# Optimization experiments

Hardware: AMD Instinct MI355X
Metric: run time of the kernel (lower is better)

## Reference

```python
import jax, jax.numpy as jnp
import numpy as np

B, CIN, COUT = 2, 64, 64
D, H, W = 8, 32, 32
KD = KH = KW = 3
K = KD * KH * KW  # 27
STRIDE, PAD, DIL = 1, 1, 1
DOUT = (D + 2 * PAD - DIL * (KD - 1) - 1) // STRIDE + 1
HOUT = (H + 2 * PAD - DIL * (KH - 1) - 1) // STRIDE + 1
WOUT = (W + 2 * PAD - DIL * (KW - 1) - 1) // STRIDE + 1


def setup_inputs() -> dict:
    key = jax.random.key(0)
    k1, k2, k3, k4 = jax.random.split(key, 4)
    x = jax.random.normal(k1, (B, CIN, D, H, W), dtype=jnp.float32)
    offset = jax.random.normal(k2, (B, 3 * K, DOUT, HOUT, WOUT), dtype=jnp.float32)
    weight = jax.random.normal(k3, (COUT, CIN, KD, KH, KW), dtype=jnp.float32) * 0.05
    bias = jax.random.normal(k4, (COUT,), dtype=jnp.float32) * 0.1
    return {"x": x, "offset": offset, "weight": weight, "bias": bias}


def _trilinear_sample(xb, zd, zh, zw):
    # xb: [C, D, H, W]; zd/zh/zw: [K, P] float sampling coords (zero padding outside)
    Dd, Hh, Ww = xb.shape[1], xb.shape[2], xb.shape[3]
    d0 = jnp.floor(zd); h0 = jnp.floor(zh); w0 = jnp.floor(zw)
    fd = zd - d0; fh = zh - h0; fw = zw - w0
    d0i = d0.astype(jnp.int32); h0i = h0.astype(jnp.int32); w0i = w0.astype(jnp.int32)
    acc = jnp.zeros((xb.shape[0],) + zd.shape, dtype=xb.dtype)
    for dd in (0, 1):
        for dh in (0, 1):
            for dw in (0, 1):
                di = d0i + dd; hi = h0i + dh; wi = w0i + dw
                wgt = ((fd if dd else 1.0 - fd) * (fh if dh else 1.0 - fh)
                       * (fw if dw else 1.0 - fw))
                valid = ((di >= 0) & (di < Dd) & (hi >= 0) & (hi < Hh)
                         & (wi >= 0) & (wi < Ww)).astype(xb.dtype)
                v = xb[:, jnp.clip(di, 0, Dd - 1), jnp.clip(hi, 0, Hh - 1),
                       jnp.clip(wi, 0, Ww - 1)]  # [C, K, P]
                acc = acc + v * (wgt * valid)[None]
    return acc


def _deform_conv3d(x, offset, weight, bias):
    Bb = x.shape[0]
    P = DOUT * HOUT * WOUT
    # kernel taps
    kd, kh, kw = jnp.unravel_index(jnp.arange(K), (KD, KH, KW))
    # output grid
    od, oh, ow = jnp.meshgrid(jnp.arange(DOUT), jnp.arange(HOUT), jnp.arange(WOUT), indexing="ij")
    base_d = (od[None] * STRIDE - PAD + kd[:, None, None, None] * DIL).astype(jnp.float32)  # [K,Do,Ho,Wo]
    base_h = (oh[None] * STRIDE - PAD + kh[:, None, None, None] * DIL).astype(jnp.float32)
    base_w = (ow[None] * STRIDE - PAD + kw[:, None, None, None] * DIL).astype(jnp.float32)
    off = offset.reshape(Bb, K, 3, DOUT, HOUT, WOUT)  # per-tap (dd, dh, dw)
    zd = (base_d[None] + off[:, :, 0]).reshape(Bb, K, P)
    zh = (base_h[None] + off[:, :, 1]).reshape(Bb, K, P)
    zw = (base_w[None] + off[:, :, 2]).reshape(Bb, K, P)
    sampled = jax.vmap(_trilinear_sample)(x, zd, zh, zw)  # [B, C, K, P]
    wmat = weight.reshape(COUT, CIN, K)
    out = jnp.einsum("bckp,ock->bop", sampled, wmat)  # [B, COUT, P]
    out = out + bias[None, :, None]
    return out.reshape(Bb, COUT, DOUT, HOUT, WOUT)


def reference(x, offset, weight, bias):
    return _deform_conv3d(x, offset, weight, bias)
```

## Files before the change

### kernel.cpp

```cpp
#include <hip/hip_runtime.h>
#include <hip/hip_bf16.h>


#define BB    2
#define CINC  64
#define COUTC 64
#define DDEP  8
#define HGT   32
#define WID   32
#define KK    27
#define KGRP  9
#define KPB   3
#define PP    8192
#define TP    64
#define LDW   72

typedef short s16x8 __attribute__((ext_vector_type(8)));
typedef float f32x4 __attribute__((ext_vector_type(4)));
typedef unsigned short u16x8 __attribute__((ext_vector_type(8)));

__device__ __forceinline__ unsigned short f2bf(float f) {
    unsigned u = __builtin_bit_cast(unsigned, f);
    u += 0x7FFFu + ((u >> 16) & 1u);
    return (unsigned short)(u >> 16);
}

__device__ __forceinline__ unsigned pack2bf(float lo, float hi) {
    return (unsigned)f2bf(lo) | ((unsigned)f2bf(hi) << 16);
}

__device__ __forceinline__ float bfu_lo(unsigned v) {
    return __builtin_bit_cast(float, v << 16);
}
__device__ __forceinline__ float bfu_hi(unsigned v) {
    return __builtin_bit_cast(float, v & 0xFFFF0000u);
}

__global__ void pre_kernel(const float* __restrict__ x, const float* __restrict__ w,
                           unsigned short* __restrict__ xt, unsigned short* __restrict__ wt) {
    __shared__ float sT[64][65];
    const int t    = threadIdx.x;
    const int lane = t & 63;
    const int wv   = t >> 6;
    const int half = lane >> 5;
    const int c2   = lane & 31;
    int blk = blockIdx.x;
    if (blk < 256) {
        int b  = blk >> 7;
        int s0 = (blk & 127) * 64;
        #pragma unroll
        for (int i = 0; i < 16; ++i) {
            int c = wv * 16 + i;
            sT[c][lane] = x[(size_t)(b * CINC + c) * PP + s0 + lane];
        }
        __syncthreads();
        #pragma unroll
        for (int i = 0; i < 8; ++i) {
            int s = wv * 16 + 2 * i + half;
            unsigned pk = pack2bf(sT[2 * c2][s], sT[2 * c2 + 1][s]);
            *(unsigned*)&xt[(size_t)(b * PP + s0 + s) * 64 + 2 * c2] = pk;
        }
    } else {
        int id = (blk - 256) * 256 + t;
        if (id < KK * COUTC * CINC) {
            int c = id & 63;
            int o = (id >> 6) & 63;
            int k = id >> 12;
            wt[id] = f2bf(w[(o * CINC + c) * KK + k]);
        }
    }
}

__device__ __forceinline__ void acc8(float* s, int4 v, float wg) {
    s[0] += wg * bfu_lo((unsigned)v.x); s[1] += wg * bfu_hi((unsigned)v.x);
    s[2] += wg * bfu_lo((unsigned)v.y); s[3] += wg * bfu_hi((unsigned)v.y);
    s[4] += wg * bfu_lo((unsigned)v.z); s[5] += wg * bfu_hi((unsigned)v.z);
    s[6] += wg * bfu_lo((unsigned)v.w); s[7] += wg * bfu_hi((unsigned)v.w);
}

__global__ __launch_bounds__(256, 3) void deform_kernel(
    const unsigned short* __restrict__ xt, const float* __restrict__ off,
    const unsigned short* __restrict__ wt, const float* __restrict__ bias,
    float* __restrict__ out)
{
    __shared__ unsigned short sW[KPB * COUTC * LDW] __attribute__((aligned(16)));
    __shared__ unsigned short sS[TP * LDW]          __attribute__((aligned(16)));
    __shared__ u16x8 sIdx[KPB][TP] __attribute__((aligned(16)));
    __shared__ float sCf[KPB][TP][8] __attribute__((aligned(16)));

    const int t    = threadIdx.x;
    const int lane = t & 63;
    const int wv   = t >> 6;
    const int b    = blockIdx.x >> 7;
    const int p0   = (blockIdx.x & 127) * TP;
    const int kg   = blockIdx.y;

    const unsigned short* xb = xt + (size_t)b * PP * 64;

    f32x4 acc[4];
    #pragma unroll
    for (int f = 0; f < 4; ++f) acc[f] = (f32x4)0.0f;

    const int n0 = lane & 15;
    const int q  = lane >> 4;

    {
        const unsigned short* wk = wt + (kg * KPB) * (COUTC * CINC);
        #pragma unroll
        for (int j = 0; j < 6; ++j) {
            int idx = j * 2048 + t * 8;
            int kl  = idx >> 12;
            int rem = idx & 4095;
            *(s16x8*)&sW[kl * (COUTC * LDW) + (rem >> 6) * LDW + (rem & 63)] =
                *(const s16x8*)(wk + idx);
        }
    }

    if (t < KPB * TP) {
        int kl = t >> 6;
        int k  = kg * KPB + kl;
        int pl = t & 63;
        int pp = p0 + pl;
        int ow = pp & 31;
        int oh = (pp >> 5) & 31;
        int od = pp >> 10;
        int kd = k / 9;
        int kh = (k - kd * 9) / 3;
        int kw = k - kd * 9 - kh * 3;
        const float* ob = off + (size_t)(b * (3 * KK) + 3 * k) * PP + pp;
        float zd = (float)(od - 1 + kd) + ob[0];
        float zh = (float)(oh - 1 + kh) + ob[PP];
        float zw = (float)(ow - 1 + kw) + ob[2 * PP];

        float fdf = floorf(zd); int d0 = (int)fdf; float fd = zd - fdf;
        float fhf = floorf(zh); int h0 = (int)fhf; float fh = zh - fhf;
        float fwf = floorf(zw); int w0 = (int)fwf; float fw = zw - fwf;

        float Bd0 = (d0 >= 0     && d0 < DDEP)     ? 1.0f - fd : 0.0f;
        float Bd1 = (d0 + 1 >= 0 && d0 + 1 < DDEP) ? fd        : 0.0f;
        float Ch0 = (h0 >= 0     && h0 < HGT)      ? 1.0f - fh : 0.0f;
        float Ch1 = (h0 + 1 >= 0 && h0 + 1 < HGT)  ? fh        : 0.0f;
        float Aw0 = (w0 >= 0     && w0 < WID)      ? 1.0f - fw : 0.0f;
        float Aw1 = (w0 + 1 >= 0 && w0 + 1 < WID)  ? fw        : 0.0f;
        int dc0 = min(max(d0, 0), DDEP - 1);
        int dc1 = min(max(d0 + 1, 0), DDEP - 1);
        int hc0 = min(max(h0, 0), HGT - 1);
        int hc1 = min(max(h0 + 1, 0), HGT - 1);
        int wc0 = min(max(w0, 0), WID - 1);
        int wc1 = min(max(w0 + 1, 0), WID - 1);

        int dh0 = (dc0 * HGT + hc0) * WID;
        int dh1 = (dc0 * HGT + hc1) * WID;
        int dh2 = (dc1 * HGT + hc0) * WID;
        int dh3 = (dc1 * HGT + hc1) * WID;
        u16x8 iv;
        iv[0] = (unsigned short)(dh0 + wc0);
        iv[1] = (unsigned short)(dh1 + wc0);
        iv[2] = (unsigned short)(dh2 + wc0);
        iv[3] = (unsigned short)(dh3 + wc0);
        iv[4] = (unsigned short)(dh0 + wc1);
        iv[5] = (unsigned short)(dh1 + wc1);
        iv[6] = (unsigned short)(dh2 + wc1);
        iv[7] = (unsigned short)(dh3 + wc1);
        sIdx[kl][pl] = iv;
        float bc0 = Bd0 * Ch0, bc1 = Bd0 * Ch1, bc2 = Bd1 * Ch0, bc3 = Bd1 * Ch1;
        sCf[kl][pl][0] = bc0 * Aw0;
        sCf[kl][pl][1] = bc1 * Aw0;
        sCf[kl][pl][2] = bc2 * Aw0;
        sCf[kl][pl][3] = bc3 * Aw0;
        sCf[kl][pl][4] = bc0 * Aw1;
        sCf[kl][pl][5] = bc1 * Aw1;
        sCf[kl][pl][6] = bc2 * Aw1;
        sCf[kl][pl][7] = bc3 * Aw1;
    }
    __syncthreads();

    const int coff = (lane & 7) * 8;
    #pragma unroll 1
    for (int kl = 0; kl < KPB; ++kl) {
        #pragma unroll
        for (int jp = 0; jp < 2; ++jp) {
            int prow = 16 * wv + 8 * jp + (lane >> 3);
            u16x8  iv = sIdx[kl][prow];
            float4 u0 = *(const float4*)&sCf[kl][prow][0];
            float4 u1 = *(const float4*)&sCf[kl][prow][4];
            const int4 v0 = *(const int4*)(xb + ((int)iv[0] << 6) + coff);
            const int4 v1 = *(const int4*)(xb + ((int)iv[1] << 6) + coff);
            const int4 v2 = *(const int4*)(xb + ((int)iv[2] << 6) + coff);
            const int4 v3 = *(const int4*)(xb + ((int)iv[3] << 6) + coff);
            const int4 v4 = *(const int4*)(xb + ((int)iv[4] << 6) + coff);
            const int4 v5 = *(const int4*)(xb + ((int)iv[5] << 6) + coff);
            const int4 v6 = *(const int4*)(xb + ((int)iv[6] << 6) + coff);
            const int4 v7 = *(const int4*)(xb + ((int)iv[7] << 6) + coff);
            float s[8] = {0, 0, 0, 0, 0, 0, 0, 0};
            acc8(s, v0, u0.x);
            acc8(s, v1, u0.y);
            acc8(s, v2, u0.z);
            acc8(s, v3, u0.w);
            acc8(s, v4, u1.x);
            acc8(s, v5, u1.y);
            acc8(s, v6, u1.z);
            acc8(s, v7, u1.w);
            int4 pk;
            pk.x = (int)pack2bf(s[0], s[1]);
            pk.y = (int)pack2bf(s[2], s[3]);
            pk.z = (int)pack2bf(s[4], s[5]);
            pk.w = (int)pack2bf(s[6], s[7]);
            *(int4*)&sS[prow * LDW + coff] = pk;
        }
        {
            s16x8 b0 = *(const s16x8*)&sS[(16 * wv + n0) * LDW +      8 * q];
            s16x8 b1 = *(const s16x8*)&sS[(16 * wv + n0) * LDW + 32 + 8 * q];
            const unsigned short* sWk = &sW[kl * (COUTC * LDW)];
            #pragma unroll
            for (int f = 0; f < 4; ++f) {
                s16x8 a0 = *(const s16x8*)&sWk[(16 * f + n0) * LDW +      8 * q];
                s16x8 a1 = *(const s16x8*)&sWk[(16 * f + n0) * LDW + 32 + 8 * q];
                acc[f] = __builtin_amdgcn_mfma_f32_16x16x32_bf16(a0, b0, acc[f], 0, 0, 0);
                acc[f] = __builtin_amdgcn_mfma_f32_16x16x32_bf16(a1, b1, acc[f], 0, 0, 0);
            }
        }
    }

    const int pdst = p0 + 16 * wv + n0;
    #pragma unroll
    for (int f = 0; f < 4; ++f) {
        #pragma unroll
        for (int r = 0; r < 4; ++r) {
            int o = 16 * f + 4 * q + r;
            float add = acc[f][r] + ((kg == 0) ? bias[o] : 0.0f);
            unsafeAtomicAdd(&out[(size_t)(b * COUTC + o) * PP + pdst], add);
        }
    }
}

extern "C" void kernel_launch(void* const* d_in, const int* in_sizes, int n_in,
                              void* d_out, int out_size, void* d_ws, size_t ws_size,
                              hipStream_t stream) {
    const float* x    = (const float*)d_in[0];
    const float* off  = (const float*)d_in[1];
    const float* w    = (const float*)d_in[2];
    const float* bias = (const float*)d_in[3];
    float* out        = (float*)d_out;

    unsigned short* xt = (unsigned short*)d_ws;
    unsigned short* wt = (unsigned short*)((char*)d_ws + (size_t)BB * PP * 64 * 2);

    (void)hipMemsetAsync(out, 0, (size_t)out_size * sizeof(float), stream);
    hipLaunchKernelGGL(pre_kernel, dim3(256 + (KK * COUTC * CINC + 255) / 256), dim3(256), 0,
                       stream, x, w, xt, wt);
    hipLaunchKernelGGL(deform_kernel, dim3(BB * (PP / TP), KGRP), dim3(256), 0, stream,
                       xt, off, wt, bias, out);
}
```

Measured before the change: 111.7 us.

## Use single-wave blocks with register-held weights, dropping shared weight staging

The deform kernel moves from 256-thread blocks covering 64 points to 64-thread single-wave blocks covering 16 points, which quadruples the grid. Weight fragments are now loaded straight from global memory into registers for each tap rather than staged in shared memory, and the __syncthreads calls are removed since one wave owns its shared data. The bilinear accumulation is rewritten as packed float2 operations so the compiler can emit packed FMA. The aim is to remove LDS weight staging and block barriers and to raise occupancy, at the cost of every block re-reading weights from global or L2.

```diff
diff --git a/kernel.cpp b/kernel.cpp
--- a/kernel.cpp
+++ b/kernel.cpp
@@ -12,11 +12,12 @@
 #define KGRP  9
 #define KPB   3
 #define PP    8192
-#define TP    64
+#define TPW   16
 #define LDW   72
 
 typedef short s16x8 __attribute__((ext_vector_type(8)));
 typedef float f32x4 __attribute__((ext_vector_type(4)));
+typedef float f32x2 __attribute__((ext_vector_type(2)));
 typedef unsigned short u16x8 __attribute__((ext_vector_type(8)));
 
 __device__ __forceinline__ unsigned short f2bf(float f) {
@@ -29,11 +30,11 @@
     return (unsigned)f2bf(lo) | ((unsigned)f2bf(hi) << 16);
 }
 
-__device__ __forceinline__ float bfu_lo(unsigned v) {
-    return __builtin_bit_cast(float, v << 16);
-}
-__device__ __forceinline__ float bfu_hi(unsigned v) {
-    return __builtin_bit_cast(float, v & 0xFFFF0000u);
+__device__ __forceinline__ f32x2 bfu2(unsigned v) {
+    f32x2 r;
+    r.x = __builtin_bit_cast(float, v << 16);
+    r.y = __builtin_bit_cast(float, v & 0xFFFF0000u);
+    return r;
 }
 
 __global__ void pre_kernel(const float* __restrict__ x, const float* __restrict__ w,
@@ -71,28 +72,26 @@
     }
 }
 
-__device__ __forceinline__ void acc8(float* s, int4 v, float wg) {
-    s[0] += wg * bfu_lo((unsigned)v.x); s[1] += wg * bfu_hi((unsigned)v.x);
-    s[2] += wg * bfu_lo((unsigned)v.y); s[3] += wg * bfu_hi((unsigned)v.y);
-    s[4] += wg * bfu_lo((unsigned)v.z); s[5] += wg * bfu_hi((unsigned)v.z);
-    s[6] += wg * bfu_lo((unsigned)v.w); s[7] += wg * bfu_hi((unsigned)v.w);
-}
-
-__global__ __launch_bounds__(256, 3) void deform_kernel(
+__device__ __forceinline__ void acc4pk(f32x2* s2, int4 v, float wg) {
+    f32x2 wg2; wg2.x = wg; wg2.y = wg;
+    s2[0] += wg2 * bfu2((unsigned)v.x);
+    s2[1] += wg2 * bfu2((unsigned)v.y);
+    s2[2] += wg2 * bfu2((unsigned)v.z);
+    s2[3] += wg2 * bfu2((unsigned)v.w);
+}
+
+__global__ __launch_bounds__(64, 4) void deform_kernel(
     const unsigned short* __restrict__ xt, const float* __restrict__ off,
     const unsigned short* __restrict__ wt, const float* __restrict__ bias,
     float* __restrict__ out)
 {
-    __shared__ unsigned short sW[KPB * COUTC * LDW] __attribute__((aligned(16)));
-    __shared__ unsigned short sS[TP * LDW]          __attribute__((aligned(16)));
-    __shared__ u16x8 sIdx[KPB][TP] __attribute__((aligned(16)));
-    __shared__ float sCf[KPB][TP][8] __attribute__((aligned(16)));
-
-    const int t    = threadIdx.x;
-    const int lane = t & 63;
-    const int wv   = t >> 6;
-    const int b    = blockIdx.x >> 7;
-    const int p0   = (blockIdx.x & 127) * TP;
+    __shared__ unsigned short sS[TPW * LDW] __attribute__((aligned(16)));
+    __shared__ u16x8 sIdx[KPB][TPW] __attribute__((aligned(16)));
+    __shared__ float sCf[KPB][TPW][8] __attribute__((aligned(16)));
+
+    const int lane = threadIdx.x;
+    const int b    = blockIdx.x >> 9;
+    const int p0   = (blockIdx.x & 511) * TPW;
     const int kg   = blockIdx.y;
 
     const unsigned short* xb = xt + (size_t)b * PP * 64;
@@ -104,22 +103,10 @@
     const int n0 = lane & 15;
     const int q  = lane >> 4;
 
-    {
-        const unsigned short* wk = wt + (kg * KPB) * (COUTC * CINC);
-        #pragma unroll
-        for (int j = 0; j < 6; ++j) {
-            int idx = j * 2048 + t * 8;
-            int kl  = idx >> 12;
-            int rem = idx & 4095;
-            *(s16x8*)&sW[kl * (COUTC * LDW) + (rem >> 6) * LDW + (rem & 63)] =
-                *(const s16x8*)(wk + idx);
-        }
-    }
-
-    if (t < KPB * TP) {
-        int kl = t >> 6;
+    if (lane < KPB * TPW) {
+        int kl = lane >> 4;
         int k  = kg * KPB + kl;
-        int pl = t & 63;
+        int pl = lane & 15;
         int pp = p0 + pl;
         int ow = pp & 31;
         int oh = (pp >> 5) & 31;
@@ -162,7 +149,7 @@
         iv[5] = (unsigned short)(dh1 + wc1);
         iv[6] = (unsigned short)(dh2 + wc1);
         iv[7] = (unsigned short)(dh3 + wc1);
-        sIdx[kl][pl] = iv;
+        sIdx[kl][lane & 15] = iv;
         float bc0 = Bd0 * Ch0, bc1 = Bd0 * Ch1, bc2 = Bd1 * Ch0, bc3 = Bd1 * Ch1;
         sCf[kl][pl][0] = bc0 * Aw0;
         sCf[kl][pl][1] = bc1 * Aw0;
@@ -173,56 +160,67 @@
         sCf[kl][pl][6] = bc2 * Aw1;
         sCf[kl][pl][7] = bc3 * Aw1;
     }
-    __syncthreads();
-
+
+    const unsigned short* xbc = xb + (lane & 7) * 8;
     const int coff = (lane & 7) * 8;
-    #pragma unroll 1
+
+    #pragma unroll
     for (int kl = 0; kl < KPB; ++kl) {
+        const int k = kg * KPB + kl;
+        const unsigned short* wk = wt + k * (COUTC * CINC) + n0 * 64 + 8 * q;
+
+        s16x8 wf[4][2];
+        #pragma unroll
+        for (int f = 0; f < 4; ++f) {
+            wf[f][0] = *(const s16x8*)(wk + f * 1024);
+            wf[f][1] = *(const s16x8*)(wk + f * 1024 + 32);
+        }
+
         #pragma unroll
         for (int jp = 0; jp < 2; ++jp) {
-            int prow = 16 * wv + 8 * jp + (lane >> 3);
+            int prow = 8 * jp + (lane >> 3);
             u16x8  iv = sIdx[kl][prow];
             float4 u0 = *(const float4*)&sCf[kl][prow][0];
             float4 u1 = *(const float4*)&sCf[kl][prow][4];
-            const int4 v0 = *(const int4*)(xb + ((int)iv[0] << 6) + coff);
-            const int4 v1 = *(const int4*)(xb + ((int)iv[1] << 6) + coff);
-            const int4 v2 = *(const int4*)(xb + ((int)iv[2] << 6) + coff);
-            const int4 v3 = *(const int4*)(xb + ((int)iv[3] << 6) + coff);
-            const int4 v4 = *(const int4*)(xb + ((int)iv[4] << 6) + coff);
-            const int4 v5 = *(const int4*)(xb + ((int)iv[5] << 6) + coff);
-            const int4 v6 = *(const int4*)(xb + ((int)iv[6] << 6) + coff);
-            const int4 v7 = *(const int4*)(xb + ((int)iv[7] << 6) + coff);
-            float s[8] = {0, 0, 0, 0, 0, 0, 0, 0};
-            acc8(s, v0, u0.x);
-            acc8(s, v1, u0.y);
-            acc8(s, v2, u0.z);
-            acc8(s, v3, u0.w);
-            acc8(s, v4, u1.x);
-            acc8(s, v5, u1.y);
-            acc8(s, v6, u1.z);
-            acc8(s, v7, u1.w);
+            const int4 v0 = *(const int4*)(xbc + ((int)iv[0] << 6));
+            const int4 v1 = *(const int4*)(xbc + ((int)iv[1] << 6));
+            const int4 v2 = *(const int4*)(xbc + ((int)iv[2] << 6));
+            const int4 v3 = *(const int4*)(xbc + ((int)iv[3] << 6));
+            const int4 v4 = *(const int4*)(xbc + ((int)iv[4] << 6));
+            const int4 v5 = *(const int4*)(xbc + ((int)iv[5] << 6));
+            const int4 v6 = *(const int4*)(xbc + ((int)iv[6] << 6));
+            const int4 v7 = *(const int4*)(xbc + ((int)iv[7] << 6));
+            f32x2 s2[4];
+            #pragma unroll
+            for (int j = 0; j < 4; ++j) { s2[j].x = 0.0f; s2[j].y = 0.0f; }
+            acc4pk(s2, v0, u0.x);
+            acc4pk(s2, v1, u0.y);
+            acc4pk(s2, v2, u0.z);
+            acc4pk(s2, v3, u0.w);
+            acc4pk(s2, v4, u1.x);
+            acc4pk(s2, v5, u1.y);
+            acc4pk(s2, v6, u1.z);
+            acc4pk(s2, v7, u1.w);
             int4 pk;
-            pk.x = (int)pack2bf(s[0], s[1]);
-            pk.y = (int)pack2bf(s[2], s[3]);
-            pk.z = (int)pack2bf(s[4], s[5]);
-            pk.w = (int)pack2bf(s[6], s[7]);
+            pk.x = (int)pack2bf(s2[0].x, s2[0].y);
+            pk.y = (int)pack2bf(s2[1].x, s2[1].y);
+            pk.z = (int)pack2bf(s2[2].x, s2[2].y);
+            pk.w = (int)pack2bf(s2[3].x, s2[3].y);
             *(int4*)&sS[prow * LDW + coff] = pk;
         }
+
         {
-            s16x8 b0 = *(const s16x8*)&sS[(16 * wv + n0) * LDW +      8 * q];
-            s16x8 b1 = *(const s16x8*)&sS[(16 * wv + n0) * LDW + 32 + 8 * q];
-            const unsigned short* sWk = &sW[kl * (COUTC * LDW)];
+            s16x8 b0 = *(const s16x8*)&sS[n0 * LDW +      8 * q];
+            s16x8 b1 = *(const s16x8*)&sS[n0 * LDW + 32 + 8 * q];
             #pragma unroll
             for (int f = 0; f < 4; ++f) {
-                s16x8 a0 = *(const s16x8*)&sWk[(16 * f + n0) * LDW +      8 * q];
-                s16x8 a1 = *(const s16x8*)&sWk[(16 * f + n0) * LDW + 32 + 8 * q];
-                acc[f] = __builtin_amdgcn_mfma_f32_16x16x32_bf16(a0, b0, acc[f], 0, 0, 0);
-                acc[f] = __builtin_amdgcn_mfma_f32_16x16x32_bf16(a1, b1, acc[f], 0, 0, 0);
+                acc[f] = __builtin_amdgcn_mfma_f32_16x16x32_bf16(wf[f][0], b0, acc[f], 0, 0, 0);
+                acc[f] = __builtin_amdgcn_mfma_f32_16x16x32_bf16(wf[f][1], b1, acc[f], 0, 0, 0);
             }
         }
     }
 
-    const int pdst = p0 + 16 * wv + n0;
+    const int pdst = p0 + n0;
     #pragma unroll
     for (int f = 0; f < 4; ++f) {
         #pragma unroll
@@ -249,6 +247,6 @@
     (void)hipMemsetAsync(out, 0, (size_t)out_size * sizeof(float), stream);
     hipLaunchKernelGGL(pre_kernel, dim3(256 + (KK * COUTC * CINC + 255) / 256), dim3(256), 0,
                        stream, x, w, xt, wt);
-    hipLaunchKernelGGL(deform_kernel, dim3(BB * (PP / TP), KGRP), dim3(256), 0, stream,
+    hipLaunchKernelGGL(deform_kernel, dim3(BB * (PP / TPW), KGRP), dim3(64), 0, stream,
                        xt, off, wt, bias, out);
 }
```

Result: slower. 125.0 us (+12.0%).
